# Kernel optimization log

Measured on AMD Instinct MI355X. Metric: run time of the kernel, lower is better.

## Reference

```python
import jax, jax.numpy as jnp
import numpy as np

H, KV, Dh = 16, 4, 128
ROPE_BASE = 10000.0


def _rope(x, pos):
    # x: (B, nh, T, Dh); pos: (T,)
    inv = 1.0 / (ROPE_BASE ** (jnp.arange(0, Dh, 2, dtype=jnp.float32) / Dh))  # (Dh/2,)
    freqs = pos.astype(jnp.float32)[:, None] * inv[None, :]                    # (T, Dh/2)
    cos = jnp.cos(freqs).astype(x.dtype)[None, None]                           # (1,1,T,Dh/2)
    sin = jnp.sin(freqs).astype(x.dtype)[None, None]
    x1, x2 = x[..., ::2], x[..., 1::2]
    o1 = x1 * cos - x2 * sin
    o2 = x1 * sin + x2 * cos
    return jnp.stack([o1, o2], axis=-1).reshape(x.shape)


def setup_inputs() -> dict:
    key = jax.random.key(0)
    ks = jax.random.split(key, 5)
    B, T, d = 2, 2048, 2048
    s = 1.0 / np.sqrt(d)
    return {
        "x": jax.random.normal(ks[0], (B, T, d), dtype=jnp.float32),
        "Wq": jax.random.normal(ks[1], (d, H * Dh), dtype=jnp.float32) * s,
        "Wk": jax.random.normal(ks[2], (d, KV * Dh), dtype=jnp.float32) * s,
        "Wv": jax.random.normal(ks[3], (d, KV * Dh), dtype=jnp.float32) * s,
        "Wo": jax.random.normal(ks[4], (H * Dh, d), dtype=jnp.float32) * s,
    }


def reference(x, Wq, Wk, Wv, Wo):
    B, T, d = x.shape
    rep = H // KV
    q = (x @ Wq).reshape(B, T, H, Dh).transpose(0, 2, 1, 3)   # (B,H,T,Dh)
    k = (x @ Wk).reshape(B, T, KV, Dh).transpose(0, 2, 1, 3)  # (B,KV,T,Dh)
    v = (x @ Wv).reshape(B, T, KV, Dh).transpose(0, 2, 1, 3)

    pos = jnp.arange(T)
    q = _rope(q, pos)
    k = _rope(k, pos)

    # GQA repeat_kv: (B,KV,T,Dh) -> (B,H,T,Dh), heads repeated consecutively
    k_full = jnp.repeat(k, rep, axis=1)
    v_full = jnp.repeat(v, rep, axis=1)

    scale = 1.0 / np.sqrt(Dh)
    scores = jnp.einsum('bhqd,bhkd->bhqk', q, k_full) * scale  # (B,H,T,T)
    causal = jnp.tril(jnp.ones((T, T), dtype=bool))
    scores = jnp.where(causal[None, None], scores, -jnp.inf)
    attn = jax.nn.softmax(scores, axis=-1)
    out = jnp.einsum('bhqk,bhkd->bhqd', attn, v_full)          # (B,H,T,Dh)
    out = out.transpose(0, 2, 1, 3).reshape(B, T, H * Dh)
    return out @ Wo
```

## Files before the change

kernel.cpp:

```cpp
#include <hip/hip_runtime.h>
#include <stdint.h>

typedef __bf16 bf16;
typedef __bf16 bf16x8 __attribute__((ext_vector_type(8)));
typedef __bf16 bf16x4 __attribute__((ext_vector_type(4)));
typedef float  f32x4  __attribute__((ext_vector_type(4)));

#define T_SEQ  2048
#define NHEAD  16
#define DHEAD  128
#define DMODEL 2048
#define NQKV   3072
#define UNROLL _Pragma("unroll")

__device__ __forceinline__ void gload_lds16(const void* g, void* l) {
  __builtin_amdgcn_global_load_lds(
      (const __attribute__((address_space(1))) uint32_t*)g,
      (__attribute__((address_space(3))) uint32_t*)l, 16, 0, 0);
}

__device__ __forceinline__ void twt_body(const float* __restrict__ W,
                                         bf16* __restrict__ WT, int K, int N,
                                         int bx, int by, float (*t)[65]) {
  int k0 = bx * 64, n0 = by * 64;
  int r4 = threadIdx.x >> 6, c = threadIdx.x & 63;
#pragma unroll
  for (int i = 0; i < 16; i++) {
    int r = i * 4 + r4;
    t[r][c] = W[(size_t)(k0 + r) * N + n0 + c];
  }
  __syncthreads();
#pragma unroll
  for (int i = 0; i < 16; i++) {
    int r = i * 4 + r4;
    WT[(size_t)(n0 + r) * K + k0 + c] = (bf16)t[c][r];
  }
}

__global__ __launch_bounds__(256) void k_prep(const float* __restrict__ x,
                                              const float* __restrict__ Wq,
                                              const float* __restrict__ Wk,
                                              const float* __restrict__ Wv,
                                              const float* __restrict__ Wo,
                                              bf16* __restrict__ xb,
                                              bf16* __restrict__ WT,
                                              bf16* __restrict__ WoT) {
  __shared__ float t[64][65];
  const int blk = blockIdx.x;
  if (blk < 8192) {
    int i = (blk * 256 + threadIdx.x) * 4;
    float4 v = *(const float4*)(x + i);
    bf16x4 o = { (bf16)v.x, (bf16)v.y, (bf16)v.z, (bf16)v.w };
    *(bf16x4*)(xb + i) = o;
  } else if (blk < 9216) {
    int b = blk - 8192;
    twt_body(Wq, WT, 2048, 2048, b & 31, b >> 5, t);
  } else if (blk < 9472) {
    int b = blk - 9216;
    twt_body(Wk, WT + (size_t)2048 * 2048, 2048, 512, b & 31, b >> 5, t);
  } else if (blk < 9728) {
    int b = blk - 9472;
    twt_body(Wv, WT + (size_t)2560 * 2048, 2048, 512, b & 31, b >> 5, t);
  } else {
    int b = blk - 9728;
    twt_body(Wo, WoT, 2048, 2048, b & 31, b >> 5, t);
  }
}

__global__ __launch_bounds__(256) void k_post(bf16* __restrict__ QKV,
                                              bf16* __restrict__ Vtg) {
  __shared__ bf16 t[64][65];
  const int blk = blockIdx.x;
  if (blk < 5120) {
    const float L2B = 0.20762050593046007f;
    int tid = blk * 256 + threadIdx.x;
    int row = tid / 320;
    int c8 = (tid - row * 320) * 8;
    int tt = row & (T_SEQ - 1);
    bf16* p = QKV + (size_t)row * NQKV + c8;
    bf16x8 v = *(const bf16x8*)p;
    int ib = (c8 & 127) >> 1;
    bf16x8 o;
#pragma unroll
    for (int m = 0; m < 4; m++) {
      float inv = exp2f(-(float)(ib + m) * L2B);
      float ang = (float)tt * inv;
      float cs, sn;
      __sincosf(ang, &sn, &cs);
      float x1 = (float)v[2 * m], x2 = (float)v[2 * m + 1];
      o[2 * m]     = (bf16)(x1 * cs - x2 * sn);
      o[2 * m + 1] = (bf16)(x1 * sn + x2 * cs);
    }
    *(bf16x8*)p = o;
  } else {
    int bb = blk - 5120;
    int bx = bb & 31, by = (bb >> 5) & 1, g = bb >> 6;
    const int t0 = bx * 64, d0 = by * 64;
    const int b = g >> 2, kvh = g & 3;
    const bf16* src = QKV + (size_t)b * T_SEQ * NQKV + 2560 + kvh * DHEAD;
    bf16* dst = Vtg + ((size_t)(b * 4 + kvh) * 128 + d0) * T_SEQ + t0;
    const int r4 = threadIdx.x >> 6, c = threadIdx.x & 63;
#pragma unroll
    for (int i = 0; i < 16; i++) {
      int r = i * 4 + r4;
      t[r][c] = src[(size_t)(t0 + r) * NQKV + d0 + c];
    }
    __syncthreads();
#pragma unroll
    for (int i = 0; i < 16; i++) {
      int r = i * 4 + r4;
      dst[(size_t)r * T_SEQ + c] = t[c][r];
    }
  }
}

#define PH(BUF, P, RB, VMW, STAGE) do {                                                   \
    bf16x8 a0k0 = rdA(BUF, 2*(P),     0), a0k1 = rdA(BUF, 2*(P),     1);                  \
    bf16x8 a1k0 = rdA(BUF, 2*(P) + 1, 0), a1k1 = rdA(BUF, 2*(P) + 1, 1);                  \
    if (RB) {                                                                             \
      UNROLL for (int n = 0; n < 4; n++) { b0[n] = rdB(BUF, 0, n); b1[n] = rdB(BUF, 1, n); } \
    }                                                                                     \
    STAGE                                                                                 \
    __builtin_amdgcn_sched_barrier(0);                                                    \
    __builtin_amdgcn_s_barrier();                                                         \
    asm volatile("s_waitcnt lgkmcnt(0)" ::: "memory");                                    \
    __builtin_amdgcn_sched_barrier(0);                                                    \
    __builtin_amdgcn_s_setprio(1);                                                        \
    UNROLL for (int n = 0; n < 4; n++) {                                                  \
      acc[2*(P)][n]   = __builtin_amdgcn_mfma_f32_16x16x32_bf16(a0k0, b0[n], acc[2*(P)][n], 0, 0, 0);     \
      acc[2*(P)][n]   = __builtin_amdgcn_mfma_f32_16x16x32_bf16(a0k1, b1[n], acc[2*(P)][n], 0, 0, 0);     \
      acc[2*(P)+1][n] = __builtin_amdgcn_mfma_f32_16x16x32_bf16(a1k0, b0[n], acc[2*(P)+1][n], 0, 0, 0);   \
      acc[2*(P)+1][n] = __builtin_amdgcn_mfma_f32_16x16x32_bf16(a1k1, b1[n], acc[2*(P)+1][n], 0, 0, 0);   \
    }                                                                                     \
    __builtin_amdgcn_s_setprio(0);                                                        \
    if (VMW) { asm volatile("s_waitcnt vmcnt(4)" ::: "memory"); }                         \
    __builtin_amdgcn_sched_barrier(0);                                                    \
    __builtin_amdgcn_s_barrier();                                                         \
  } while (0)

template<bool F32OUT>
__global__ __launch_bounds__(512) void k_gemm2(const bf16* __restrict__ A,
                                               const bf16* __restrict__ BT,
                                               void* __restrict__ C,
                                               int M, int N, int K) {
  __shared__ __align__(16) bf16 L[2][2][2][8192];
  const int nwg = gridDim.x * gridDim.y;
  const int orig = blockIdx.y * gridDim.x + blockIdx.x;
  const int tile = (orig & 7) * (nwg >> 3) + (orig >> 3);
  const int m0 = (tile % gridDim.x) * 256, n0 = (tile / gridDim.x) * 256;
  const int tid = threadIdx.x;
  const int lane = tid & 63, w = tid >> 6;
  const int wr = w >> 2, wc = w & 3;
  const int l15 = lane & 15, lg = lane >> 4;
  const int srow = tid >> 3;
  const int scol = ((tid & 7) ^ (srow & 7)) * 8;
  const int NKT = K >> 6;

  f32x4 acc[8][4] = {};
  bf16x8 b0[4], b1[4];

  auto stA = [&](int buf, int half, int kt) {
    const bf16* g = A + (size_t)(m0 + half * 128 + srow) * K + kt * 64 + scol;
    bf16* lb = &L[buf][0][half][w * 512];
    gload_lds16(g, lb);
    gload_lds16(g + (size_t)64 * K, lb + 4096);
  };
  auto stB = [&](int buf, int half, int kt) {
    const bf16* g = BT + (size_t)(n0 + half * 128 + srow) * K + kt * 64 + scol;
    bf16* lb = &L[buf][1][half][w * 512];
    gload_lds16(g, lb);
    gload_lds16(g + (size_t)64 * K, lb + 4096);
  };
  auto rdA = [&](int buf, int fr, int kk) -> bf16x8 {
    int r = fr * 16 + l15;
    return *(const bf16x8*)((const char*)&L[buf][0][wr][0] + r * 128 +
                            (((kk * 4 + lg) ^ (r & 7)) << 4));
  };
  auto rdB = [&](int buf, int kk, int n) -> bf16x8 {
    int rr = wc * 64 + n * 16 + l15;
    return *(const bf16x8*)((const char*)&L[buf][1][rr >> 7][0] + (rr & 127) * 128 +
                            (((kk * 4 + lg) ^ (rr & 7)) << 4));
  };

  stA(0, 0, 0); stA(0, 1, 0);
  stB(0, 0, 0); stB(0, 1, 0);
  stB(1, 0, 1); stB(1, 1, 1);
  asm volatile("s_waitcnt vmcnt(4)" ::: "memory");
  __builtin_amdgcn_sched_barrier(0);
  __builtin_amdgcn_s_barrier();

  for (int it = 0; it < (NKT >> 1); ++it) {
    const int t1 = 2 * it + 1;
    const int t2 = (t1 + 1 < NKT) ? t1 + 1 : NKT - 1;
    const int t3 = (t1 + 2 < NKT) ? t1 + 2 : NKT - 1;
    PH(0, 0, 1, 0, stA(1, 0, t1););
    PH(0, 1, 0, 0, stA(1, 1, t1););
    PH(0, 2, 0, 0, stB(0, 0, t2););
    PH(0, 3, 0, 1, stB(0, 1, t2););
    PH(1, 0, 1, 0, stA(0, 0, t2););
    PH(1, 1, 0, 0, stA(0, 1, t2););
    PH(1, 2, 0, 0, stB(1, 0, t3););
    PH(1, 3, 0, 1, stB(1, 1, t3););
  }

  const int r0 = m0 + wr * 128 + lg * 4;
  const int c0 = n0 + wc * 64 + l15;
  UNROLL for (int m = 0; m < 8; m++)
    UNROLL for (int n = 0; n < 4; n++)
      UNROLL for (int i = 0; i < 4; i++) {
        size_t idx = (size_t)(r0 + m * 16 + i) * N + (c0 + n * 16);
        if (F32OUT) ((float*)C)[idx] = acc[m][n][i];
        else        ((bf16*)C)[idx]  = (bf16)acc[m][n][i];
      }
}

#define PH2(BUF, P, RB, VMW, STAGE) do {                                                  \
    bf16x8 a0k0 = rdA(BUF, 2*(P),     0), a0k1 = rdA(BUF, 2*(P),     1);                  \
    bf16x8 a1k0 = rdA(BUF, 2*(P) + 1, 0), a1k1 = rdA(BUF, 2*(P) + 1, 1);                  \
    if (RB) {                                                                             \
      UNROLL for (int n = 0; n < 2; n++) { b0[n] = rdB(BUF, 0, n); b1[n] = rdB(BUF, 1, n); } \
    }                                                                                     \
    STAGE                                                                                 \
    __builtin_amdgcn_sched_barrier(0);                                                    \
    __builtin_amdgcn_s_barrier();                                                         \
    asm volatile("s_waitcnt lgkmcnt(0)" ::: "memory");                                    \
    __builtin_amdgcn_sched_barrier(0);                                                    \
    __builtin_amdgcn_s_setprio(1);                                                        \
    UNROLL for (int n = 0; n < 2; n++) {                                                  \
      acc[2*(P)][n]   = __builtin_amdgcn_mfma_f32_16x16x32_bf16(a0k0, b0[n], acc[2*(P)][n], 0, 0, 0);     \
      acc[2*(P)][n]   = __builtin_amdgcn_mfma_f32_16x16x32_bf16(a0k1, b1[n], acc[2*(P)][n], 0, 0, 0);     \
      acc[2*(P)+1][n] = __builtin_amdgcn_mfma_f32_16x16x32_bf16(a1k0, b0[n], acc[2*(P)+1][n], 0, 0, 0);   \
      acc[2*(P)+1][n] = __builtin_amdgcn_mfma_f32_16x16x32_bf16(a1k1, b1[n], acc[2*(P)+1][n], 0, 0, 0);   \
    }                                                                                     \
    __builtin_amdgcn_s_setprio(0);                                                        \
    if (VMW) { asm volatile("s_waitcnt vmcnt(2)" ::: "memory"); }                         \
    __builtin_amdgcn_sched_barrier(0);                                                    \
    __builtin_amdgcn_s_barrier();                                                         \
  } while (0)

__global__ __launch_bounds__(512) void k_gemm3(const bf16* __restrict__ A,
                                               const bf16* __restrict__ BT,
                                               float* __restrict__ C,
                                               int M, int N, int K) {
  __shared__ __align__(16) bf16 L[2][3][8192];
  const int nwg = gridDim.x * gridDim.y;
  const int orig = blockIdx.y * gridDim.x + blockIdx.x;
  const int tile = (orig & 7) * (nwg >> 3) + (orig >> 3);
  const int m0 = (tile % gridDim.x) * 256, n0 = (tile / gridDim.x) * 128;
  const int tid = threadIdx.x;
  const int lane = tid & 63, w = tid >> 6;
  const int wr = w >> 2, wc = w & 3;
  const int l15 = lane & 15, lg = lane >> 4;
  const int srow = tid >> 3;
  const int scol = ((tid & 7) ^ (srow & 7)) * 8;
  const int NKT = K >> 6;

  f32x4 acc[8][2] = {};
  bf16x8 b0[2], b1[2];

  auto stA = [&](int buf, int half, int kt) {
    const bf16* g = A + (size_t)(m0 + half * 128 + srow) * K + kt * 64 + scol;
    bf16* lb = &L[buf][half][w * 512];
    gload_lds16(g, lb);
    gload_lds16(g + (size_t)64 * K, lb + 4096);
  };
  auto stB = [&](int buf, int kt) {
    const bf16* g = BT + (size_t)(n0 + srow) * K + kt * 64 + scol;
    bf16* lb = &L[buf][2][w * 512];
    gload_lds16(g, lb);
    gload_lds16(g + (size_t)64 * K, lb + 4096);
  };
  auto rdA = [&](int buf, int fr, int kk) -> bf16x8 {
    int r = fr * 16 + l15;
    return *(const bf16x8*)((const char*)&L[buf][wr][0] + r * 128 +
                            (((kk * 4 + lg) ^ (r & 7)) << 4));
  };
  auto rdB = [&](int buf, int kk, int n) -> bf16x8 {
    int rr = wc * 32 + n * 16 + l15;
    return *(const bf16x8*)((const char*)&L[buf][2][0] + rr * 128 +
                            (((kk * 4 + lg) ^ (rr & 7)) << 4));
  };

  stA(0, 0, 0); stA(0, 1, 0); stB(0, 0);
  stB(1, 1);
  asm volatile("s_waitcnt vmcnt(2)" ::: "memory");
  __builtin_amdgcn_sched_barrier(0);
  __builtin_amdgcn_s_barrier();

  for (int it = 0; it < (NKT >> 1); ++it) {
    const int t1 = 2 * it + 1;
    const int t2 = (t1 + 1 < NKT) ? t1 + 1 : NKT - 1;
    const int t3 = (t1 + 2 < NKT) ? t1 + 2 : NKT - 1;
    PH2(0, 0, 1, 0, stA(1, 0, t1););
    PH2(0, 1, 0, 0, stA(1, 1, t1););
    PH2(0, 2, 0, 0, stB(0, t2););
    PH2(0, 3, 0, 1, ;);
    PH2(1, 0, 1, 0, stA(0, 0, t2););
    PH2(1, 1, 0, 0, stA(0, 1, t2););
    PH2(1, 2, 0, 0, stB(1, t3););
    PH2(1, 3, 0, 1, ;);
  }

  const int r0 = m0 + wr * 128 + lg * 4;
  const int c0 = n0 + wc * 32 + l15;
  UNROLL for (int m = 0; m < 8; m++)
    UNROLL for (int n = 0; n < 2; n++)
      UNROLL for (int i = 0; i < 4; i++)
        C[(size_t)(r0 + m * 16 + i) * N + (c0 + n * 16)] = acc[m][n][i];
}

#define COMPUTE2(kt) do {                                                                 \
    f32x4 sA_[4] = {}, sB_[4] = {};                                                       \
    const char* ks_ = (const char*)Ks;                                                    \
    __builtin_amdgcn_s_setprio(1);                                                        \
    UNROLL for (int kk = 0; kk < 4; kk++)                                                 \
      UNROLL for (int n = 0; n < 4; n++) {                                                \
        int row_ = n * 16 + l15;                                                          \
        int cb_ = (kk * 64 + lg * 16) ^ ((row_ & 7) << 4);                                \
        bf16x8 kf_ = *(const bf16x8*)(ks_ + row_ * 256 + cb_);                            \
        sA_[n] = __builtin_amdgcn_mfma_f32_16x16x32_bf16(kf_, qA[kk], sA_[n], 0, 0, 0);   \
        sB_[n] = __builtin_amdgcn_mfma_f32_16x16x32_bf16(kf_, qB[kk], sB_[n], 0, 0, 0);   \
      }                                                                                   \
    __builtin_amdgcn_s_setprio(0);                                                        \
    __syncthreads();                               \
    if ((kt) + 1 < NT) issueK((kt) + 1);                \
    float vmA_ = -1e30f, vmB_ = -1e30f;                                                   \
    if ((kt) == qt) {                                                                     \
      UNROLL for (int n = 0; n < 4; n++)                                                  \
        UNROLL for (int i = 0; i < 4; i++) {                                              \
          if ((kt) * 64 + n * 16 + lg * 4 + i > qglob) {                                  \
            sA_[n][i] = -1e30f; sB_[n][i] = -1e30f;                                       \
          }                                                                               \
          vmA_ = fmaxf(vmA_, sA_[n][i]);                                                  \
          vmB_ = fmaxf(vmB_, sB_[n][i]);                                                  \
        }                                                                                 \
    } else {                                                                              \
      UNROLL for (int n = 0; n < 4; n++)                                                  \
        UNROLL for (int i = 0; i < 4; i++) {                                              \
          vmA_ = fmaxf(vmA_, sA_[n][i]);                                                  \
          vmB_ = fmaxf(vmB_, sB_[n][i]);                                                  \
        }                                                                                 \
    }                                                                                     \
    vmA_ = fmaxf(vmA_, __shfl_xor(vmA_, 16));                                             \
    vmA_ = fmaxf(vmA_, __shfl_xor(vmA_, 32));                                             \
    vmB_ = fmaxf(vmB_, __shfl_xor(vmB_, 16));                                             \
    vmB_ = fmaxf(vmB_, __shfl_xor(vmB_, 32));                                             \
    if (!__all((vmA_ <= mA + 8.0f) && (vmB_ <= mB + 8.0f))) {                             \
      float mnA_ = fmaxf(mA, vmA_), mnB_ = fmaxf(mB, vmB_);                               \
      float alA_ = __builtin_amdgcn_exp2f(mA - mnA_);                                     \
      float alB_ = __builtin_amdgcn_exp2f(mB - mnB_);                                     \
      mA = mnA_; mB = mnB_;                                                               \
      lA *= alA_; lB *= alB_;                                                             \
      UNROLL for (int i = 0; i < 4; i++) {                                                \
        int src_ = (lane & 48) + ((lane >> 2) & 12) + i;                                  \
        float aA_ = __shfl(alA_, src_);                                                   \
        float aB_ = __shfl(alB_, src_);                                                   \
        UNROLL for (int n = 0; n < 8; n++) { oA[n][i] *= aA_; oB[n][i] *= aB_; }          \
      }                                                                                   \
    }                                                                                     \
    bf16x8 paA0_, paA1_, paB0_, paB1_;                                                    \
    {                                                                                     \
      float rs_ = 0.f;                                                                    \
      UNROLL for (int n = 0; n < 4; n++) {                                                \
        bf16x4 pk_;                                                                       \
        UNROLL for (int i = 0; i < 4; i++) {                                              \
          float pv_ = __builtin_amdgcn_exp2f(sA_[n][i] - mA);                             \
          rs_ += pv_;                                                                     \
          pk_[i] = (bf16)pv_;                                                             \
        }                                                                                 \
        *(bf16x4*)(&Ps[w][l15][n * 16 + lg * 4]) = pk_;                                   \
      }                                                                                   \
      rs_ += __shfl_xor(rs_, 16);                                                         \
      rs_ += __shfl_xor(rs_, 32);                                                         \
      lA += rs_;                                                                          \
      paA0_ = *(const bf16x8*)(&Ps[w][l15][lg * 8]);                                      \
      paA1_ = *(const bf16x8*)(&Ps[w][l15][32 + lg * 8]);                                 \
    }                                                                                     \
    {                                                                                     \
      float rs_ = 0.f;                                                                    \
      UNROLL for (int n = 0; n < 4; n++) {                                                \
        bf16x4 pk_;                                                                       \
        UNROLL for (int i = 0; i < 4; i++) {                                              \
          float pv_ = __builtin_amdgcn_exp2f(sB_[n][i] - mB);                             \
          rs_ += pv_;                                                                     \
          pk_[i] = (bf16)pv_;                                                             \
        }                                                                                 \
        *(bf16x4*)(&Ps[w][l15][n * 16 + lg * 4]) = pk_;                                   \
      }                                                                                   \
      rs_ += __shfl_xor(rs_, 16);                                                         \
      rs_ += __shfl_xor(rs_, 32);                                                         \
      lB += rs_;                                                                          \
      paB0_ = *(const bf16x8*)(&Ps[w][l15][lg * 8]);                                      \
      paB1_ = *(const bf16x8*)(&Ps[w][l15][32 + lg * 8]);                                 \
    }                                                                                     \
    const char* vs_ = (const char*)Vs;                                                    \
    __builtin_amdgcn_s_setprio(1);                                                        \
    UNROLL for (int n = 0; n < 8; n++) {                                                  \
      int d_ = n * 16 + l15;                                                              \
      bf16x8 vf0_ = *(const bf16x8*)(vs_ + d_ * 128 + (((lg) ^ (d_ & 7)) << 4));          \
      oA[n] = __builtin_amdgcn_mfma_f32_16x16x32_bf16(paA0_, vf0_, oA[n], 0, 0, 0);       \
      oB[n] = __builtin_amdgcn_mfma_f32_16x16x32_bf16(paB0_, vf0_, oB[n], 0, 0, 0);       \
      bf16x8 vf1_ = *(const bf16x8*)(vs_ + d_ * 128 + (((4 + lg) ^ (d_ & 7)) << 4));      \
      oA[n] = __builtin_amdgcn_mfma_f32_16x16x32_bf16(paA1_, vf1_, oA[n], 0, 0, 0);       \
      oB[n] = __builtin_amdgcn_mfma_f32_16x16x32_bf16(paB1_, vf1_, oB[n], 0, 0, 0);       \
    }                                                                                     \
    __builtin_amdgcn_s_setprio(0);                                                        \
    __syncthreads();                             \
    if ((kt) + 1 < NT) issueV((kt) + 1);              \
  } while (0)

__global__ __launch_bounds__(256) void k_flash(const bf16* __restrict__ QKV,
                                               const bf16* __restrict__ Vtg,
                                               bf16* __restrict__ AO) {
  __shared__ __align__(16) bf16 Ks[64 * 128];
  __shared__ __align__(16) bf16 Vs[128 * 64];
  __shared__ __align__(16) bf16 Ps[4][16][72];
  const int orig = blockIdx.y * 32 + blockIdx.x;
  const int fin  = ((orig & 7) << 6) | (orig >> 3);
  const int bhp  = fin >> 5;
  const int qt   = 31 - (fin & 31);
  const int b = bhp >> 3, kvh = (bhp >> 1) & 3, hp = bhp & 1;
  const int h0 = kvh * 4 + hp * 2, h1 = h0 + 1;
  const int tid = threadIdx.x, lane = tid & 63, w = tid >> 6;
  const int l15 = lane & 15, lg = lane >> 4;
  const int qglob = qt * 64 + w * 16 + l15;
  const float qs = 0.12753102f;

  bf16x8 qA[4], qB[4];
  {
    const size_t qoA = (size_t)(b * T_SEQ + qt * 64 + w * 16 + l15) * NQKV + h0 * DHEAD;
    const size_t qoB = (size_t)(b * T_SEQ + qt * 64 + w * 16 + l15) * NQKV + h1 * DHEAD;
    UNROLL for (int kk = 0; kk < 4; kk++) {
      bf16x8 a = *(const bf16x8*)(QKV + qoA + kk * 32 + lg * 8);
      bf16x8 bb = *(const bf16x8*)(QKV + qoB + kk * 32 + lg * 8);
      UNROLL for (int j = 0; j < 8; j++) {
        a[j] = (bf16)((float)a[j] * qs);
        bb[j] = (bf16)((float)bb[j] * qs);
      }
      qA[kk] = a; qB[kk] = bb;
    }
  }

  f32x4 oA[8] = {}, oB[8] = {};
  float mA = -1e30f, mB = -1e30f, lA = 0.f, lB = 0.f;

  const bf16* Kbase = QKV + (size_t)b * T_SEQ * NQKV + DMODEL + kvh * DHEAD;
  const bf16* Vbase = Vtg + (size_t)(b * 4 + kvh) * 128 * T_SEQ;

  auto issueK = [&](int kt) {
    UNROLL for (int i = 0; i < 4; i++) {
      int row = w * 16 + i * 4 + lg;
      int col = (l15 ^ (row & 7)) * 8;
      gload_lds16(Kbase + (size_t)(kt * 64 + row) * NQKV + col,
                  Ks + (w * 4 + i) * 512);
    }
  };
  auto issueV = [&](int kt) {
    UNROLL for (int i = 0; i < 4; i++) {
      int d = (w * 4 + i) * 8 + (lane >> 3);
      int u = lane & 7;
      gload_lds16(Vbase + (size_t)d * T_SEQ + kt * 64 + ((u ^ (d & 7)) * 8),
                  Vs + (w * 4 + i) * 512);
    }
  };

  issueK(0);
  issueV(0);
  __syncthreads();

  const int NT = qt + 1;
  for (int kt = 0; kt < NT; kt++) {
    COMPUTE2(kt);
  }

  {
    const size_t ob0 = (size_t)(b * T_SEQ + qt * 64 + w * 16 + lg * 4) * DMODEL + h0 * DHEAD + l15;
    const size_t ob1 = (size_t)(b * T_SEQ + qt * 64 + w * 16 + lg * 4) * DMODEL + h1 * DHEAD + l15;
    UNROLL for (int i = 0; i < 4; i++) {
      int src = (lane & 48) + ((lane >> 2) & 12) + i;
      float invA = 1.0f / __shfl(lA, src);
      float invB = 1.0f / __shfl(lB, src);
      UNROLL for (int n = 0; n < 8; n++) {
        AO[ob0 + (size_t)i * DMODEL + n * 16] = (bf16)(oA[n][i] * invA);
        AO[ob1 + (size_t)i * DMODEL + n * 16] = (bf16)(oB[n][i] * invB);
      }
    }
  }
}

extern "C" void kernel_launch(void* const* d_in, const int* in_sizes, int n_in,
                              void* d_out, int out_size, void* d_ws, size_t ws_size,
                              hipStream_t stream) {
  const float* x  = (const float*)d_in[0];
  const float* Wq = (const float*)d_in[1];
  const float* Wk = (const float*)d_in[2];
  const float* Wv = (const float*)d_in[3];
  const float* Wo = (const float*)d_in[4];
  char* ws = (char*)d_ws;
  bf16* xb  = (bf16*)ws;
  bf16* WT  = (bf16*)(ws + 16777216ull);
  bf16* WoT = (bf16*)(ws + 16777216ull + 12582912ull);
  bf16* QKV = (bf16*)(ws + 16777216ull + 12582912ull + 8388608ull);
  bf16* AO  = (bf16*)(ws + 16777216ull + 12582912ull + 8388608ull + 25165824ull);
  bf16* Vtg = WT;
  float* out = (float*)d_out;

  k_prep<<<10752, 256, 0, stream>>>(x, Wq, Wk, Wv, Wo, xb, WT, WoT);
  k_gemm2<false><<<dim3(16, 12), 512, 0, stream>>>(xb, WT, QKV, 4096, 3072, 2048);
  k_post<<<5632, 256, 0, stream>>>(QKV, Vtg);
  k_flash<<<dim3(32, 16), 256, 0, stream>>>(QKV, Vtg, AO);
  k_gemm3<<<dim3(16, 16), 512, 0, stream>>>(AO, WoT, out, 4096, 2048, 2048);
}
```

Before: 196.6 us.

## Retile QKV GEMM to 128x384 tiles to fill all CUs

Replaces the 256x256-tile QKV projection GEMM with a 128x384-tile variant launched on a 32x8 grid, so the workgroup count matches the CU count instead of leaving some CUs idle. Each warp now holds a 4x6 accumulator block, and the LDS staging is reorganised into one A tile plus three B chunks with adjusted wait counts. The intent is to remove wave-quantization idle time, at the cost of a narrower M tile and slightly less operand reuse per loaded byte.

```diff
diff --git a/kernel.cpp b/kernel.cpp
--- a/kernel.cpp
+++ b/kernel.cpp
@@ -114,11 +114,10 @@
   }
 }
 
-#define PH(BUF, P, RB, VMW, STAGE) do {                                                   \
-    bf16x8 a0k0 = rdA(BUF, 2*(P),     0), a0k1 = rdA(BUF, 2*(P),     1);                  \
-    bf16x8 a1k0 = rdA(BUF, 2*(P) + 1, 0), a1k1 = rdA(BUF, 2*(P) + 1, 1);                  \
+#define PHQ(BUF, P, RB, VMW, STAGE) do {                                                  \
+    bf16x8 ak0 = rdA(BUF, P, 0), ak1 = rdA(BUF, P, 1);                                    \
     if (RB) {                                                                             \
-      UNROLL for (int n = 0; n < 4; n++) { b0[n] = rdB(BUF, 0, n); b1[n] = rdB(BUF, 1, n); } \
+      UNROLL for (int n = 0; n < 6; n++) { b0[n] = rdB(BUF, 0, n); b1[n] = rdB(BUF, 1, n); } \
     }                                                                                     \
     STAGE                                                                                 \
     __builtin_amdgcn_sched_barrier(0);                                                    \
@@ -126,28 +125,25 @@
     asm volatile("s_waitcnt lgkmcnt(0)" ::: "memory");                                    \
     __builtin_amdgcn_sched_barrier(0);                                                    \
     __builtin_amdgcn_s_setprio(1);                                                        \
-    UNROLL for (int n = 0; n < 4; n++) {                                                  \
-      acc[2*(P)][n]   = __builtin_amdgcn_mfma_f32_16x16x32_bf16(a0k0, b0[n], acc[2*(P)][n], 0, 0, 0);     \
-      acc[2*(P)][n]   = __builtin_amdgcn_mfma_f32_16x16x32_bf16(a0k1, b1[n], acc[2*(P)][n], 0, 0, 0);     \
-      acc[2*(P)+1][n] = __builtin_amdgcn_mfma_f32_16x16x32_bf16(a1k0, b0[n], acc[2*(P)+1][n], 0, 0, 0);   \
-      acc[2*(P)+1][n] = __builtin_amdgcn_mfma_f32_16x16x32_bf16(a1k1, b1[n], acc[2*(P)+1][n], 0, 0, 0);   \
+    UNROLL for (int n = 0; n < 6; n++) {                                                  \
+      acc[P][n] = __builtin_amdgcn_mfma_f32_16x16x32_bf16(ak0, b0[n], acc[P][n], 0, 0, 0);\
+      acc[P][n] = __builtin_amdgcn_mfma_f32_16x16x32_bf16(ak1, b1[n], acc[P][n], 0, 0, 0);\
     }                                                                                     \
     __builtin_amdgcn_s_setprio(0);                                                        \
-    if (VMW) { asm volatile("s_waitcnt vmcnt(4)" ::: "memory"); }                         \
+    if (VMW) { asm volatile("s_waitcnt vmcnt(6)" ::: "memory"); }                         \
     __builtin_amdgcn_sched_barrier(0);                                                    \
     __builtin_amdgcn_s_barrier();                                                         \
   } while (0)
 
-template<bool F32OUT>
-__global__ __launch_bounds__(512) void k_gemm2(const bf16* __restrict__ A,
+__global__ __launch_bounds__(512) void k_gemmQ(const bf16* __restrict__ A,
                                                const bf16* __restrict__ BT,
-                                               void* __restrict__ C,
+                                               bf16* __restrict__ C,
                                                int M, int N, int K) {
-  __shared__ __align__(16) bf16 L[2][2][2][8192];
+  __shared__ __align__(16) bf16 L[2][4][8192];
   const int nwg = gridDim.x * gridDim.y;
   const int orig = blockIdx.y * gridDim.x + blockIdx.x;
   const int tile = (orig & 7) * (nwg >> 3) + (orig >> 3);
-  const int m0 = (tile % gridDim.x) * 256, n0 = (tile / gridDim.x) * 256;
+  const int m0 = (tile % gridDim.x) * 128, n0 = (tile / gridDim.x) * 384;
   const int tid = threadIdx.x;
   const int lane = tid & 63, w = tid >> 6;
   const int wr = w >> 2, wc = w & 3;
@@ -156,36 +152,36 @@
   const int scol = ((tid & 7) ^ (srow & 7)) * 8;
   const int NKT = K >> 6;
 
-  f32x4 acc[8][4] = {};
-  bf16x8 b0[4], b1[4];
-
-  auto stA = [&](int buf, int half, int kt) {
-    const bf16* g = A + (size_t)(m0 + half * 128 + srow) * K + kt * 64 + scol;
-    bf16* lb = &L[buf][0][half][w * 512];
+  f32x4 acc[4][6] = {};
+  bf16x8 b0[6], b1[6];
+
+  auto stA = [&](int buf, int kt) {
+    const bf16* g = A + (size_t)(m0 + srow) * K + kt * 64 + scol;
+    bf16* lb = &L[buf][0][w * 512];
     gload_lds16(g, lb);
     gload_lds16(g + (size_t)64 * K, lb + 4096);
   };
-  auto stB = [&](int buf, int half, int kt) {
-    const bf16* g = BT + (size_t)(n0 + half * 128 + srow) * K + kt * 64 + scol;
-    bf16* lb = &L[buf][1][half][w * 512];
+  auto stB = [&](int buf, int c, int kt) {
+    const bf16* g = BT + (size_t)(n0 + c * 128 + srow) * K + kt * 64 + scol;
+    bf16* lb = &L[buf][1 + c][w * 512];
     gload_lds16(g, lb);
     gload_lds16(g + (size_t)64 * K, lb + 4096);
   };
-  auto rdA = [&](int buf, int fr, int kk) -> bf16x8 {
-    int r = fr * 16 + l15;
-    return *(const bf16x8*)((const char*)&L[buf][0][wr][0] + r * 128 +
+  auto rdA = [&](int buf, int m, int kk) -> bf16x8 {
+    int r = wr * 64 + m * 16 + l15;
+    return *(const bf16x8*)((const char*)&L[buf][0][0] + r * 128 +
                             (((kk * 4 + lg) ^ (r & 7)) << 4));
   };
   auto rdB = [&](int buf, int kk, int n) -> bf16x8 {
-    int rr = wc * 64 + n * 16 + l15;
-    return *(const bf16x8*)((const char*)&L[buf][1][rr >> 7][0] + (rr & 127) * 128 +
+    int rr = wc * 96 + n * 16 + l15;
+    return *(const bf16x8*)((const char*)&L[buf][1 + (rr >> 7)][0] + (rr & 127) * 128 +
                             (((kk * 4 + lg) ^ (rr & 7)) << 4));
   };
 
-  stA(0, 0, 0); stA(0, 1, 0);
-  stB(0, 0, 0); stB(0, 1, 0);
-  stB(1, 0, 1); stB(1, 1, 1);
-  asm volatile("s_waitcnt vmcnt(4)" ::: "memory");
+  stA(0, 0);
+  stB(0, 0, 0); stB(0, 1, 0); stB(0, 2, 0);
+  stB(1, 0, 1); stB(1, 1, 1); stB(1, 2, 1);
+  asm volatile("s_waitcnt vmcnt(6)" ::: "memory");
   __builtin_amdgcn_sched_barrier(0);
   __builtin_amdgcn_s_barrier();
 
@@ -193,25 +189,22 @@
     const int t1 = 2 * it + 1;
     const int t2 = (t1 + 1 < NKT) ? t1 + 1 : NKT - 1;
     const int t3 = (t1 + 2 < NKT) ? t1 + 2 : NKT - 1;
-    PH(0, 0, 1, 0, stA(1, 0, t1););
-    PH(0, 1, 0, 0, stA(1, 1, t1););
-    PH(0, 2, 0, 0, stB(0, 0, t2););
-    PH(0, 3, 0, 1, stB(0, 1, t2););
-    PH(1, 0, 1, 0, stA(0, 0, t2););
-    PH(1, 1, 0, 0, stA(0, 1, t2););
-    PH(1, 2, 0, 0, stB(1, 0, t3););
-    PH(1, 3, 0, 1, stB(1, 1, t3););
-  }
-
-  const int r0 = m0 + wr * 128 + lg * 4;
-  const int c0 = n0 + wc * 64 + l15;
-  UNROLL for (int m = 0; m < 8; m++)
-    UNROLL for (int n = 0; n < 4; n++)
-      UNROLL for (int i = 0; i < 4; i++) {
-        size_t idx = (size_t)(r0 + m * 16 + i) * N + (c0 + n * 16);
-        if (F32OUT) ((float*)C)[idx] = acc[m][n][i];
-        else        ((bf16*)C)[idx]  = (bf16)acc[m][n][i];
-      }
+    PHQ(0, 0, 1, 0, stA(1, t1););
+    PHQ(0, 1, 0, 0, stB(0, 0, t2););
+    PHQ(0, 2, 0, 0, stB(0, 1, t2););
+    PHQ(0, 3, 0, 1, stB(0, 2, t2););
+    PHQ(1, 0, 1, 0, stA(0, t2););
+    PHQ(1, 1, 0, 0, stB(1, 0, t3););
+    PHQ(1, 2, 0, 0, stB(1, 1, t3););
+    PHQ(1, 3, 0, 1, stB(1, 2, t3););
+  }
+
+  const int r0 = m0 + wr * 64 + lg * 4;
+  const int c0 = n0 + wc * 96 + l15;
+  UNROLL for (int m = 0; m < 4; m++)
+    UNROLL for (int n = 0; n < 6; n++)
+      UNROLL for (int i = 0; i < 4; i++)
+        C[(size_t)(r0 + m * 16 + i) * N + (c0 + n * 16)] = (bf16)acc[m][n][i];
 }
 
 #define PH2(BUF, P, RB, VMW, STAGE) do {                                                  \
@@ -506,7 +499,7 @@
   float* out = (float*)d_out;
 
   k_prep<<<10752, 256, 0, stream>>>(x, Wq, Wk, Wv, Wo, xb, WT, WoT);
-  k_gemm2<false><<<dim3(16, 12), 512, 0, stream>>>(xb, WT, QKV, 4096, 3072, 2048);
+  k_gemmQ<<<dim3(32, 8), 512, 0, stream>>>(xb, WT, QKV, 4096, 3072, 2048);
   k_post<<<5632, 256, 0, stream>>>(QKV, Vtg);
   k_flash<<<dim3(32, 16), 256, 0, stream>>>(QKV, Vtg, AO);
   k_gemm3<<<dim3(16, 16), 512, 0, stream>>>(AO, WoT, out, 4096, 2048, 2048);
```

After: 191.6 us. 1.03x faster.
